# Kernel tuning notes

Measured on AMD Instinct MI355X. Metric: run time of the kernel, lower is better.

The kernel has to match this reference:

```python
import jax, jax.numpy as jnp
import numpy as np

C = 512

def _conv1x1(x, w, b):
    # x: [B, C, T], w: [O, C], b: [O] -> [B, O, T]
    return jnp.einsum('oc,bct->bot', w, x) + b[None, :, None]

def setup_inputs() -> dict:
    key = jax.random.key(0)
    ks = jax.random.split(key, 9)
    B, T = 8, 2048
    s = 1.0 / np.sqrt(C)
    inp = {'x': jax.random.normal(ks[0], (B, C, T), dtype=jnp.float32)}
    names = ['theta', 'phi', 'g', 'w']
    for i, n in enumerate(names):
        inp[f'w_{n}'] = jax.random.uniform(ks[1 + 2 * i], (C, C), jnp.float32, -s, s)
        inp[f'b_{n}'] = jax.random.uniform(ks[2 + 2 * i], (C,), jnp.float32, -s, s)
    return inp

def reference(x, w_theta, b_theta, w_phi, b_phi, w_g, b_g, w_w, b_w):
    relu = jax.nn.relu
    feat_theta = relu(_conv1x1(x, w_theta, b_theta))          # [B, C, T]
    feat_phi = relu(_conv1x1(x, w_phi, b_phi))                # [B, C, T]
    # scores: Q^T K over channel dim -> [B, T, T]
    scores = jnp.einsum('bci,bcj->bij', feat_theta, feat_phi)
    attn = jax.nn.softmax(scores, axis=2)                     # [B, T, T]
    feat_g = relu(_conv1x1(x, w_g, b_g))                      # [B, C, T]
    # attention-weighted V: [B, T, T] x [B, T, C] -> [B, T, C] -> [B, C, T]
    feature = jnp.einsum('bij,bcj->bci', attn, feat_g)
    w_feature = relu(_conv1x1(feature, w_w, b_w))
    return w_feature + x
```

## Files before the change

### kernel.cpp

```cpp
#include <hip/hip_runtime.h>
#include <math.h>

#define C_DIM 512
#define T_DIM 2048
#define B_DIM 8

typedef _Float16 f16;
typedef __attribute__((ext_vector_type(8))) _Float16 half8;
typedef __attribute__((ext_vector_type(4))) _Float16 half4;
typedef __attribute__((ext_vector_type(4))) float floatx4;

__global__ __launch_bounds__(256) void convert_w_kernel(
    const float* __restrict__ w0, const float* __restrict__ w1,
    const float* __restrict__ w2, const float* __restrict__ w3,
    f16* __restrict__ o0, f16* __restrict__ o1,
    f16* __restrict__ o2, f16* __restrict__ o3)
{
    const float* src; f16* dst;
    switch (blockIdx.z) {
        case 0:  src = w0; dst = o0; break;
        case 1:  src = w1; dst = o1; break;
        case 2:  src = w2; dst = o2; break;
        default: src = w3; dst = o3; break;
    }
    const int idx = (blockIdx.x * 256 + threadIdx.x) * 4;
    const float4 v = *(const float4*)(src + idx);
    half4 h; h[0] = (f16)v.x; h[1] = (f16)v.y; h[2] = (f16)v.z; h[3] = (f16)v.w;
    *(half4*)(dst + idx) = h;
}

__global__ __launch_bounds__(256) void concat_bias_kernel(
    const float* __restrict__ b0, const float* __restrict__ b1,
    float* __restrict__ o)
{
    const int i = blockIdx.x * 256 + threadIdx.x;
    o[i] = (i < 512) ? b0[i] : b1[i - 512];
}

__global__ __launch_bounds__(256) void transpose_x_kernel(
    const float* __restrict__ x, f16* __restrict__ xt)
{
    __shared__ float xs[32][33];
    const int b  = blockIdx.z;
    const int t0 = blockIdx.x * 32, c0 = blockIdx.y * 32;
    const float* xb = x + (size_t)b * C_DIM * T_DIM;
    const int r = threadIdx.x >> 3, q = threadIdx.x & 7;

    const float4 v = *(const float4*)(xb + (size_t)(c0 + r) * T_DIM + t0 + q * 4);
    xs[r][q * 4 + 0] = v.x; xs[r][q * 4 + 1] = v.y;
    xs[r][q * 4 + 2] = v.z; xs[r][q * 4 + 3] = v.w;
    __syncthreads();

    f16* xtb = xt + (size_t)b * C_DIM * T_DIM;
    half4 h;
    h[0] = (f16)xs[q * 4 + 0][r]; h[1] = (f16)xs[q * 4 + 1][r];
    h[2] = (f16)xs[q * 4 + 2][r]; h[3] = (f16)xs[q * 4 + 3][r];
    *(half4*)(xtb + (size_t)(t0 + r) * C_DIM + c0 + q * 4) = h;
}

template<int MODE>
__global__ __launch_bounds__(256) void gemm_tn(
    const f16* __restrict__ A, size_t sA, int lda,
    const f16* __restrict__ B, size_t sB, int ldb,
    void* __restrict__ Cp, size_t sC, int ldc,
    const float* __restrict__ bias,
    const float* __restrict__ resid, size_t sR,
    int K)
{
    __shared__ __align__(16) f16 As[2][128 * 32];
    __shared__ __align__(16) f16 Bs[2][128 * 32];

    const int gx = gridDim.x;
    const int flat = blockIdx.y * gx + blockIdx.x;
    const int jsc = gx >> 2;
    const int sh = (jsc <= 1) ? 0 : (31 - __builtin_clz(jsc));
    const int s = flat >> 4, rem = flat & 15;
    const int i0 = ((s >> sh) * 4 + (rem >> 2)) * 128;
    const int j0 = (((jsc <= 1) ? 0 : (s & (jsc - 1))) * 4 + (rem & 3)) * 128;

    const int bz = blockIdx.z;
    A += (size_t)bz * sA;
    B += (size_t)bz * sB;

    const int tid  = threadIdx.x;
    const int lane = tid & 63;
    const int wave = tid >> 6;
    const int wy = wave >> 1, wx = wave & 1;
    const int quad = lane >> 4, l16 = lane & 15;

    const int row1 = tid >> 2, ch = tid & 3;
    const int row2 = row1 + 64;
    const int w1 = row1 * 32 + ((ch ^ (row1 & 3)) << 3);
    const int w2 = row2 * 32 + ((ch ^ (row2 & 3)) << 3);

    const f16* gA1 = A + (size_t)(i0 + row1) * lda + ch * 8;
    const f16* gA2 = A + (size_t)(i0 + row2) * lda + ch * 8;
    const f16* gB1 = B + (size_t)(j0 + row1) * ldb + ch * 8;
    const f16* gB2 = B + (size_t)(j0 + row2) * ldb + ch * 8;

    const int xa = (quad ^ (l16 & 3)) << 3;

    const int nt = K >> 5;

    float4 a1_0 = *(const float4*)(gA1);      float4 a2_0 = *(const float4*)(gA2);
    float4 b1_0 = *(const float4*)(gB1);      float4 b2_0 = *(const float4*)(gB2);
    float4 a1_1 = *(const float4*)(gA1 + 32); float4 a2_1 = *(const float4*)(gA2 + 32);
    float4 b1_1 = *(const float4*)(gB1 + 32); float4 b2_1 = *(const float4*)(gB2 + 32);

    floatx4 acc[4][4] = {};

    for (int t = 0; t < nt; t += 2) {
        *(float4*)&As[0][w1] = a1_0;
        *(float4*)&As[0][w2] = a2_0;
        *(float4*)&Bs[0][w1] = b1_0;
        *(float4*)&Bs[0][w2] = b2_0;
        if (t + 2 < nt) {
            const int off = (t + 2) * 32;
            a1_0 = *(const float4*)(gA1 + off); a2_0 = *(const float4*)(gA2 + off);
            b1_0 = *(const float4*)(gB1 + off); b2_0 = *(const float4*)(gB2 + off);
        }
        __syncthreads();
        {
            half8 af[4], bf[4];
            #pragma unroll
            for (int mi = 0; mi < 4; ++mi)
                af[mi] = *(const half8*)&As[0][(wy * 64 + mi * 16 + l16) * 32 + xa];
            #pragma unroll
            for (int ni = 0; ni < 4; ++ni)
                bf[ni] = *(const half8*)&Bs[0][(wx * 64 + ni * 16 + l16) * 32 + xa];
            #pragma unroll
            for (int mi = 0; mi < 4; ++mi)
                #pragma unroll
                for (int ni = 0; ni < 4; ++ni)
                    acc[mi][ni] = __builtin_amdgcn_mfma_f32_16x16x32_f16(
                        af[mi], bf[ni], acc[mi][ni], 0, 0, 0);
        }
        *(float4*)&As[1][w1] = a1_1;
        *(float4*)&As[1][w2] = a2_1;
        *(float4*)&Bs[1][w1] = b1_1;
        *(float4*)&Bs[1][w2] = b2_1;
        if (t + 3 < nt) {
            const int off = (t + 3) * 32;
            a1_1 = *(const float4*)(gA1 + off); a2_1 = *(const float4*)(gA2 + off);
            b1_1 = *(const float4*)(gB1 + off); b2_1 = *(const float4*)(gB2 + off);
        }
        __syncthreads();
        {
            half8 af[4], bf[4];
            #pragma unroll
            for (int mi = 0; mi < 4; ++mi)
                af[mi] = *(const half8*)&As[1][(wy * 64 + mi * 16 + l16) * 32 + xa];
            #pragma unroll
            for (int ni = 0; ni < 4; ++ni)
                bf[ni] = *(const half8*)&Bs[1][(wx * 64 + ni * 16 + l16) * 32 + xa];
            #pragma unroll
            for (int mi = 0; mi < 4; ++mi)
                #pragma unroll
                for (int ni = 0; ni < 4; ++ni)
                    acc[mi][ni] = __builtin_amdgcn_mfma_f32_16x16x32_f16(
                        af[mi], bf[ni], acc[mi][ni], 0, 0, 0);
        }
    }

    #pragma unroll
    for (int mi = 0; mi < 4; ++mi) {
        #pragma unroll
        for (int ni = 0; ni < 4; ++ni) {
            const int col = j0 + wx * 64 + ni * 16 + l16;
            #pragma unroll
            for (int r = 0; r < 4; ++r) {
                const int row = i0 + wy * 64 + mi * 16 + quad * 4 + r;
                float v = acc[mi][ni][r];
                if (MODE == 1) { v += bias[col]; v = v > 0.f ? v : 0.f; }
                if (MODE == 2) { v += bias[row]; v = v > 0.f ? v : 0.f; }
                if (MODE == 3) {
                    v += bias[row];
                    v = v > 0.f ? v : 0.f;
                    v += resid[(size_t)bz * sR + (size_t)row * ldc + col];
                    ((float*)Cp)[(size_t)bz * sC + (size_t)row * ldc + col] = v;
                } else {
                    ((f16*)Cp)[(size_t)bz * sC + (size_t)row * ldc + col] = (f16)v;
                }
            }
        }
    }
}

__device__ __forceinline__ void gl16(const f16* g, f16* l)
{
    __builtin_amdgcn_global_load_lds(
        (const __attribute__((address_space(1))) unsigned int*)g,
        (__attribute__((address_space(3))) unsigned int*)l,
        16, 0, 0);
}

template<int MODE>
__global__ __launch_bounds__(512, 2) void gemm256(
    const f16* __restrict__ A, size_t sA, int lda,
    const f16* __restrict__ B, size_t sB, int ldb,
    void* __restrict__ Cp, size_t sC, int ldc,
    const float* __restrict__ bias,
    int K)
{
    __shared__ __align__(16) f16 As[2][2][256 * 32];
    __shared__ __align__(16) f16 Bs[2][2][256 * 32];

    const int gx = gridDim.x;
    const int flat = blockIdx.y * gx + blockIdx.x;
    const int jsc = gx >> 2;
    const int sh = (jsc <= 1) ? 0 : (31 - __builtin_clz(jsc));
    const int s = flat >> 4, rem = flat & 15;
    const int i0 = ((s >> sh) * 4 + (rem >> 2)) * 256;
    const int j0 = (((jsc <= 1) ? 0 : (s & (jsc - 1))) * 4 + (rem & 3)) * 256;

    const int bz = blockIdx.z;
    A += (size_t)bz * sA;
    B += (size_t)bz * sB;

    const int tid  = threadIdx.x;
    const int lane = tid & 63;
    const int wave = tid >> 6;
    const int wy = wave >> 2;
    const int wx = wave & 3;
    const int quad = lane >> 4, l16 = lane & 15;

    const int srow = wave * 32 + (lane >> 2);
    const int sch  = lane & 3;
    const f16* gA0 = A + (size_t)(i0 + srow) * lda + sch * 8;
    const f16* gA1 = gA0 + (size_t)16 * lda;
    const f16* gB0 = B + (size_t)(j0 + srow) * ldb + sch * 8;
    const f16* gB1 = gB0 + (size_t)16 * ldb;
    const int wsg = wave * 1024;

    const int ra = (wy * 128 + l16) * 32 + quad * 8;
    const int rb = (wx * 64 + l16) * 32 + quad * 8;

    const int nt = K >> 6;

#define STAGE_A(t, q) do {                                                    \
        const int off_ = (t) * 64 + (q) * 32;                                 \
        gl16(gA0 + off_, &As[(t) & 1][q][wsg]);                               \
        gl16(gA1 + off_, &As[(t) & 1][q][wsg + 512]);                         \
    } while (0)
#define STAGE_B(t, q) do {                                                    \
        const int off_ = (t) * 64 + (q) * 32;                                 \
        gl16(gB0 + off_, &Bs[(t) & 1][q][wsg]);                               \
        gl16(gB1 + off_, &Bs[(t) & 1][q][wsg + 512]);                         \
    } while (0)
#define PH_MFMA(B0) do {                                                      \
        __builtin_amdgcn_s_setprio(1);                                        \
        _Pragma("unroll")                                                     \
        for (int mi = 0; mi < 4; ++mi) {                                      \
            _Pragma("unroll")                                                 \
            for (int ni = 0; ni < 4; ++ni)                                    \
                acc[(B0) + mi][ni] = __builtin_amdgcn_mfma_f32_16x16x32_f16(  \
                    af[mi], bf[ni], acc[(B0) + mi][ni], 0, 0, 0);             \
        }                                                                     \
        __builtin_amdgcn_s_setprio(0);                                        \
    } while (0)

    STAGE_A(0, 0); STAGE_B(0, 0);
    STAGE_A(0, 1); STAGE_B(0, 1);
    STAGE_A(1, 0); STAGE_B(1, 0);

    floatx4 acc[8][4] = {};

    for (int t = 0; t < nt; ++t) {
        const f16* sa0 = &As[t & 1][0][0];
        const f16* sb0 = &Bs[t & 1][0][0];
        const f16* sa1 = &As[t & 1][1][0];
        const f16* sb1 = &Bs[t & 1][1][0];
        half8 af[4], bf[4];

        if (t + 1 < nt) asm volatile("s_waitcnt vmcnt(8)\ns_barrier" ::: "memory");
        else            asm volatile("s_waitcnt vmcnt(4)\ns_barrier" ::: "memory");
        #pragma unroll
        for (int ni = 0; ni < 4; ++ni) bf[ni] = *(const half8*)&sb0[rb + ni * 512];
        #pragma unroll
        for (int mi = 0; mi < 4; ++mi) af[mi] = *(const half8*)&sa0[ra + mi * 512];
        if (t + 1 < nt) STAGE_A(t + 1, 1);
        PH_MFMA(0);

        #pragma unroll
        for (int mi = 0; mi < 4; ++mi) af[mi] = *(const half8*)&sa0[ra + 2048 + mi * 512];
        if (t + 1 < nt) STAGE_B(t + 1, 1);
        PH_MFMA(4);

        if (t + 1 < nt) asm volatile("s_waitcnt vmcnt(8)\ns_barrier" ::: "memory");
        else            asm volatile("s_waitcnt vmcnt(0)\ns_barrier" ::: "memory");
        #pragma unroll
        for (int ni = 0; ni < 4; ++ni) bf[ni] = *(const half8*)&sb1[rb + ni * 512];
        #pragma unroll
        for (int mi = 0; mi < 4; ++mi) af[mi] = *(const half8*)&sa1[ra + mi * 512];
        if (t + 2 < nt) STAGE_A(t + 2, 0);
        PH_MFMA(0);

        #pragma unroll
        for (int mi = 0; mi < 4; ++mi) af[mi] = *(const half8*)&sa1[ra + 2048 + mi * 512];
        if (t + 2 < nt) STAGE_B(t + 2, 0);
        PH_MFMA(4);
    }
#undef STAGE_A
#undef STAGE_B
#undef PH_MFMA

    #pragma unroll
    for (int m = 0; m < 8; ++m) {
        #pragma unroll
        for (int ni = 0; ni < 4; ++ni) {
            const int col = j0 + wx * 64 + ni * 16 + l16;
            #pragma unroll
            for (int r = 0; r < 4; ++r) {
                const int row = i0 + wy * 128 + m * 16 + quad * 4 + r;
                float v = acc[m][ni][r];
                if (MODE == 1) { v += bias[col]; v = v > 0.f ? v : 0.f; }
                ((f16*)Cp)[(size_t)bz * sC + (size_t)row * ldc + col] = (f16)v;
            }
        }
    }
}

__global__ __launch_bounds__(256) void softmax_f16_kernel(f16* __restrict__ S)
{
    f16* p = S + (size_t)blockIdx.x * T_DIM;
    const int tid = threadIdx.x;

    half8 hv = *((const half8*)p + tid);
    float v[8];
    float lmax = -1e30f;
    #pragma unroll
    for (int c = 0; c < 8; ++c) { v[c] = (float)hv[c]; lmax = fmaxf(lmax, v[c]); }
    #pragma unroll
    for (int off = 32; off; off >>= 1)
        lmax = fmaxf(lmax, __shfl_down(lmax, off));
    __shared__ float redm[4];
    if ((tid & 63) == 0) redm[tid >> 6] = lmax;
    __syncthreads();
    const float m = fmaxf(fmaxf(redm[0], redm[1]), fmaxf(redm[2], redm[3]));

    float lsum = 0.f;
    #pragma unroll
    for (int c = 0; c < 8; ++c) { v[c] = __expf(v[c] - m); lsum += v[c]; }
    #pragma unroll
    for (int off = 32; off; off >>= 1)
        lsum += __shfl_down(lsum, off);
    __shared__ float reds[4];
    if ((tid & 63) == 0) reds[tid >> 6] = lsum;
    __syncthreads();
    const float inv = 1.f / (reds[0] + reds[1] + reds[2] + reds[3]);

    #pragma unroll
    for (int c = 0; c < 8; ++c) hv[c] = (f16)(v[c] * inv);
    *((half8*)p + tid) = hv;
}

extern "C" void kernel_launch(void* const* d_in, const int* in_sizes, int n_in,
                              void* d_out, int out_size, void* d_ws, size_t ws_size,
                              hipStream_t stream)
{
    const float* x       = (const float*)d_in[0];
    const float* w_theta = (const float*)d_in[1];
    const float* b_theta = (const float*)d_in[2];
    const float* w_phi   = (const float*)d_in[3];
    const float* b_phi   = (const float*)d_in[4];
    const float* w_g     = (const float*)d_in[5];
    const float* b_g     = (const float*)d_in[6];
    const float* w_w     = (const float*)d_in[7];
    const float* b_w     = (const float*)d_in[8];
    float* out = (float*)d_out;

    const size_t FE = (size_t)B_DIM * C_DIM * T_DIM;
    const size_t TC = (size_t)T_DIM * C_DIM;
    const size_t TT = (size_t)T_DIM * T_DIM;

    f16* xt      = (f16*)d_ws;
    f16* wtp     = xt + FE;
    f16* wg_h    = wtp + 524288;
    f16* ww_h    = wg_h + 262144;
    float* btp   = (float*)(ww_h + 262144);
    f16* tp      = (f16*)(btp + 1024);
    f16* g       = tp + (size_t)B_DIM * T_DIM * 1024;
    f16* scores  = g + FE;
    f16* feature = tp;

    const dim3 blk(256);
    const dim3 blk512(512);

    convert_w_kernel<<<dim3(256, 1, 4), blk, 0, stream>>>(
        w_theta, w_phi, w_g, w_w, wtp, wtp + 262144, wg_h, ww_h);
    concat_bias_kernel<<<dim3(4), blk, 0, stream>>>(b_theta, b_phi, btp);
    transpose_x_kernel<<<dim3(T_DIM / 32, C_DIM / 32, B_DIM), blk, 0, stream>>>(x, xt);

    gemm256<1><<<dim3(1024 / 256, T_DIM / 256, B_DIM), blk512, 0, stream>>>(
        xt, TC, C_DIM, wtp, 0, C_DIM, tp, (size_t)T_DIM * 1024, 1024,
        btp, C_DIM);
    gemm_tn<2><<<dim3(T_DIM / 128, C_DIM / 128, B_DIM), blk, 0, stream>>>(
        wg_h, 0, C_DIM, xt, TC, C_DIM, g, TC, T_DIM, b_g, nullptr, 0, C_DIM);
    gemm256<0><<<dim3(T_DIM / 256, T_DIM / 256, B_DIM), blk512, 0, stream>>>(
        tp, (size_t)T_DIM * 1024, 1024, tp + 512, (size_t)T_DIM * 1024, 1024,
        scores, TT, T_DIM, nullptr, C_DIM);
    softmax_f16_kernel<<<dim3(B_DIM * T_DIM), blk, 0, stream>>>(scores);
    gemm_tn<0><<<dim3(C_DIM / 128, T_DIM / 128, B_DIM), blk, 0, stream>>>(
        scores, TT, T_DIM, g, TC, T_DIM, feature, TC, C_DIM, nullptr, nullptr, 0, T_DIM);
    gemm_tn<3><<<dim3(T_DIM / 128, C_DIM / 128, B_DIM), blk, 0, stream>>>(
        ww_h, 0, C_DIM, feature, TC, C_DIM, out, TC, T_DIM, b_w, x, TC, C_DIM);
}
```

Measured before the change: 270.0 us.

## Replace register-staged 128x128 GEMMs with async LDS-load 128x256 kernel; wave-per-row softmax

```diff
diff --git a/kernel.cpp b/kernel.cpp
--- a/kernel.cpp
+++ b/kernel.cpp
@@ -58,8 +58,142 @@
     *(half4*)(xtb + (size_t)(t0 + r) * C_DIM + c0 + q * 4) = h;
 }
 
+__device__ __forceinline__ void gl16(const f16* g, f16* l)
+{
+    __builtin_amdgcn_global_load_lds(
+        (const __attribute__((address_space(1))) unsigned int*)g,
+        (__attribute__((address_space(3))) unsigned int*)l,
+        16, 0, 0);
+}
+
 template<int MODE>
-__global__ __launch_bounds__(256) void gemm_tn(
+__global__ __launch_bounds__(512, 2) void gemm256(
+    const f16* __restrict__ A, size_t sA, int lda,
+    const f16* __restrict__ B, size_t sB, int ldb,
+    void* __restrict__ Cp, size_t sC, int ldc,
+    const float* __restrict__ bias,
+    int K)
+{
+    __shared__ __align__(16) f16 As[2][2][256 * 32];
+    __shared__ __align__(16) f16 Bs[2][2][256 * 32];
+
+    const int gx = gridDim.x;
+    const int flat = blockIdx.y * gx + blockIdx.x;
+    const int jsc = gx >> 2;
+    const int sh = (jsc <= 1) ? 0 : (31 - __builtin_clz(jsc));
+    const int s = flat >> 4, rem = flat & 15;
+    const int i0 = ((s >> sh) * 4 + (rem >> 2)) * 256;
+    const int j0 = (((jsc <= 1) ? 0 : (s & (jsc - 1))) * 4 + (rem & 3)) * 256;
+
+    const int bz = blockIdx.z;
+    A += (size_t)bz * sA;
+    B += (size_t)bz * sB;
+
+    const int tid  = threadIdx.x;
+    const int lane = tid & 63;
+    const int wave = tid >> 6;
+    const int wy = wave >> 2;
+    const int wx = wave & 3;
+    const int quad = lane >> 4, l16 = lane & 15;
+
+    const int srow = wave * 32 + (lane >> 2);
+    const int sch  = lane & 3;
+    const f16* gA0 = A + (size_t)(i0 + srow) * lda + sch * 8;
+    const f16* gA1 = gA0 + (size_t)16 * lda;
+    const f16* gB0 = B + (size_t)(j0 + srow) * ldb + sch * 8;
+    const f16* gB1 = gB0 + (size_t)16 * ldb;
+    const int wsg = wave * 1024;
+
+    const int ra = (wy * 128 + l16) * 32 + quad * 8;
+    const int rb = (wx * 64 + l16) * 32 + quad * 8;
+
+    const int nt = K >> 6;
+
+#define STAGE_A(t, q) do {                                                    \
+        const int off_ = (t) * 64 + (q) * 32;                                 \
+        gl16(gA0 + off_, &As[(t) & 1][q][wsg]);                               \
+        gl16(gA1 + off_, &As[(t) & 1][q][wsg + 512]);                         \
+    } while (0)
+#define STAGE_B(t, q) do {                                                    \
+        const int off_ = (t) * 64 + (q) * 32;                                 \
+        gl16(gB0 + off_, &Bs[(t) & 1][q][wsg]);                               \
+        gl16(gB1 + off_, &Bs[(t) & 1][q][wsg + 512]);                         \
+    } while (0)
+#define PH_MFMA(B0) do {                                                      \
+        __builtin_amdgcn_s_setprio(1);                                        \
+        _Pragma("unroll")                                                     \
+        for (int mi = 0; mi < 4; ++mi) {                                      \
+            _Pragma("unroll")                                                 \
+            for (int ni = 0; ni < 4; ++ni)                                    \
+                acc[(B0) + mi][ni] = __builtin_amdgcn_mfma_f32_16x16x32_f16(  \
+                    af[mi], bf[ni], acc[(B0) + mi][ni], 0, 0, 0);             \
+        }                                                                     \
+        __builtin_amdgcn_s_setprio(0);                                        \
+    } while (0)
+
+    STAGE_A(0, 0); STAGE_B(0, 0);
+    STAGE_A(0, 1); STAGE_B(0, 1);
+    STAGE_A(1, 0); STAGE_B(1, 0);
+
+    floatx4 acc[8][4] = {};
+
+    for (int t = 0; t < nt; ++t) {
+        const f16* sa0 = &As[t & 1][0][0];
+        const f16* sb0 = &Bs[t & 1][0][0];
+        const f16* sa1 = &As[t & 1][1][0];
+        const f16* sb1 = &Bs[t & 1][1][0];
+        half8 af[4], bf[4];
+
+        if (t + 1 < nt) asm volatile("s_waitcnt vmcnt(8)\ns_barrier" ::: "memory");
+        else            asm volatile("s_waitcnt vmcnt(4)\ns_barrier" ::: "memory");
+        #pragma unroll
+        for (int ni = 0; ni < 4; ++ni) bf[ni] = *(const half8*)&sb0[rb + ni * 512];
+        #pragma unroll
+        for (int mi = 0; mi < 4; ++mi) af[mi] = *(const half8*)&sa0[ra + mi * 512];
+        if (t + 1 < nt) STAGE_A(t + 1, 1);
+        PH_MFMA(0);
+
+        #pragma unroll
+        for (int mi = 0; mi < 4; ++mi) af[mi] = *(const half8*)&sa0[ra + 2048 + mi * 512];
+        if (t + 1 < nt) STAGE_B(t + 1, 1);
+        PH_MFMA(4);
+
+        if (t + 1 < nt) asm volatile("s_waitcnt vmcnt(8)\ns_barrier" ::: "memory");
+        else            asm volatile("s_waitcnt vmcnt(0)\ns_barrier" ::: "memory");
+        #pragma unroll
+        for (int ni = 0; ni < 4; ++ni) bf[ni] = *(const half8*)&sb1[rb + ni * 512];
+        #pragma unroll
+        for (int mi = 0; mi < 4; ++mi) af[mi] = *(const half8*)&sa1[ra + mi * 512];
+        if (t + 2 < nt) STAGE_A(t + 2, 0);
+        PH_MFMA(0);
+
+        #pragma unroll
+        for (int mi = 0; mi < 4; ++mi) af[mi] = *(const half8*)&sa1[ra + 2048 + mi * 512];
+        if (t + 2 < nt) STAGE_B(t + 2, 0);
+        PH_MFMA(4);
+    }
+#undef STAGE_A
+#undef STAGE_B
+#undef PH_MFMA
+
+    #pragma unroll
+    for (int m = 0; m < 8; ++m) {
+        #pragma unroll
+        for (int ni = 0; ni < 4; ++ni) {
+            const int col = j0 + wx * 64 + ni * 16 + l16;
+            #pragma unroll
+            for (int r = 0; r < 4; ++r) {
+                const int row = i0 + wy * 128 + m * 16 + quad * 4 + r;
+                float v = acc[m][ni][r];
+                if (MODE == 1) { v += bias[col]; v = v > 0.f ? v : 0.f; }
+                ((f16*)Cp)[(size_t)bz * sC + (size_t)row * ldc + col] = (f16)v;
+            }
+        }
+    }
+}
+
+template<int MODE>
+__global__ __launch_bounds__(512, 2) void gemm_wide(
     const f16* __restrict__ A, size_t sA, int lda,
     const f16* __restrict__ B, size_t sB, int ldb,
     void* __restrict__ Cp, size_t sC, int ldc,
@@ -67,17 +201,11 @@
     const float* __restrict__ resid, size_t sR,
     int K)
 {
-    __shared__ __align__(16) f16 As[2][128 * 32];
-    __shared__ __align__(16) f16 Bs[2][128 * 32];
-
-    const int gx = gridDim.x;
-    const int flat = blockIdx.y * gx + blockIdx.x;
-    const int jsc = gx >> 2;
-    const int sh = (jsc <= 1) ? 0 : (31 - __builtin_clz(jsc));
-    const int s = flat >> 4, rem = flat & 15;
-    const int i0 = ((s >> sh) * 4 + (rem >> 2)) * 128;
-    const int j0 = (((jsc <= 1) ? 0 : (s & (jsc - 1))) * 4 + (rem & 3)) * 128;
-
+    __shared__ __align__(16) f16 As[2][2][128 * 32];
+    __shared__ __align__(16) f16 Bs[2][2][256 * 32];
+
+    const int i0 = blockIdx.y * 128;
+    const int j0 = blockIdx.x * 256;
     const int bz = blockIdx.z;
     A += (size_t)bz * sA;
     B += (size_t)bz * sB;
@@ -85,82 +213,73 @@
     const int tid  = threadIdx.x;
     const int lane = tid & 63;
     const int wave = tid >> 6;
-    const int wy = wave >> 1, wx = wave & 1;
+    const int wy = wave >> 2;
+    const int wx = wave & 3;
     const int quad = lane >> 4, l16 = lane & 15;
 
-    const int row1 = tid >> 2, ch = tid & 3;
-    const int row2 = row1 + 64;
-    const int w1 = row1 * 32 + ((ch ^ (row1 & 3)) << 3);
-    const int w2 = row2 * 32 + ((ch ^ (row2 & 3)) << 3);
-
-    const f16* gA1 = A + (size_t)(i0 + row1) * lda + ch * 8;
-    const f16* gA2 = A + (size_t)(i0 + row2) * lda + ch * 8;
-    const f16* gB1 = B + (size_t)(j0 + row1) * ldb + ch * 8;
-    const f16* gB2 = B + (size_t)(j0 + row2) * ldb + ch * 8;
-
-    const int xa = (quad ^ (l16 & 3)) << 3;
-
-    const int nt = K >> 5;
-
-    float4 a1_0 = *(const float4*)(gA1);      float4 a2_0 = *(const float4*)(gA2);
-    float4 b1_0 = *(const float4*)(gB1);      float4 b2_0 = *(const float4*)(gB2);
-    float4 a1_1 = *(const float4*)(gA1 + 32); float4 a2_1 = *(const float4*)(gA2 + 32);
-    float4 b1_1 = *(const float4*)(gB1 + 32); float4 b2_1 = *(const float4*)(gB2 + 32);
+    const f16* gA0 = A + (size_t)(i0 + wave * 16 + (lane >> 2)) * lda + (lane & 3) * 8;
+    const f16* gB0 = B + (size_t)(j0 + wave * 32 + (lane >> 2)) * ldb + (lane & 3) * 8;
+    const f16* gB1 = gB0 + (size_t)16 * ldb;
+
+    const int ra = (wy * 64 + l16) * 32 + quad * 8;
+    const int rb = (wx * 64 + l16) * 32 + quad * 8;
+
+    const int nt = K >> 6;
+
+#define WSTAGE_A(t, q) do {                                                   \
+        gl16(gA0 + (t) * 64 + (q) * 32, &As[(t) & 1][q][wave * 512]);         \
+    } while (0)
+#define WSTAGE_B(t, q) do {                                                   \
+        const int off_ = (t) * 64 + (q) * 32;                                 \
+        gl16(gB0 + off_, &Bs[(t) & 1][q][wave * 1024]);                       \
+        gl16(gB1 + off_, &Bs[(t) & 1][q][wave * 1024 + 512]);                 \
+    } while (0)
+#define WPH_MFMA() do {                                                       \
+        __builtin_amdgcn_s_setprio(1);                                        \
+        _Pragma("unroll")                                                     \
+        for (int mi = 0; mi < 4; ++mi) {                                      \
+            _Pragma("unroll")                                                 \
+            for (int ni = 0; ni < 4; ++ni)                                    \
+                acc[mi][ni] = __builtin_amdgcn_mfma_f32_16x16x32_f16(         \
+                    af[mi], bf[ni], acc[mi][ni], 0, 0, 0);                    \
+        }                                                                     \
+        __builtin_amdgcn_s_setprio(0);                                        \
+    } while (0)
+
+    WSTAGE_A(0, 0); WSTAGE_B(0, 0);
+    WSTAGE_A(0, 1); WSTAGE_B(0, 1);
+    WSTAGE_A(1, 0); WSTAGE_B(1, 0);
 
     floatx4 acc[4][4] = {};
 
-    for (int t = 0; t < nt; t += 2) {
-        *(float4*)&As[0][w1] = a1_0;
-        *(float4*)&As[0][w2] = a2_0;
-        *(float4*)&Bs[0][w1] = b1_0;
-        *(float4*)&Bs[0][w2] = b2_0;
-        if (t + 2 < nt) {
-            const int off = (t + 2) * 32;
-            a1_0 = *(const float4*)(gA1 + off); a2_0 = *(const float4*)(gA2 + off);
-            b1_0 = *(const float4*)(gB1 + off); b2_0 = *(const float4*)(gB2 + off);
-        }
-        __syncthreads();
-        {
-            half8 af[4], bf[4];
-            #pragma unroll
-            for (int mi = 0; mi < 4; ++mi)
-                af[mi] = *(const half8*)&As[0][(wy * 64 + mi * 16 + l16) * 32 + xa];
-            #pragma unroll
-            for (int ni = 0; ni < 4; ++ni)
-                bf[ni] = *(const half8*)&Bs[0][(wx * 64 + ni * 16 + l16) * 32 + xa];
-            #pragma unroll
-            for (int mi = 0; mi < 4; ++mi)
-                #pragma unroll
-                for (int ni = 0; ni < 4; ++ni)
-                    acc[mi][ni] = __builtin_amdgcn_mfma_f32_16x16x32_f16(
-                        af[mi], bf[ni], acc[mi][ni], 0, 0, 0);
-        }
-        *(float4*)&As[1][w1] = a1_1;
-        *(float4*)&As[1][w2] = a2_1;
-        *(float4*)&Bs[1][w1] = b1_1;
-        *(float4*)&Bs[1][w2] = b2_1;
-        if (t + 3 < nt) {
-            const int off = (t + 3) * 32;
-            a1_1 = *(const float4*)(gA1 + off); a2_1 = *(const float4*)(gA2 + off);
-            b1_1 = *(const float4*)(gB1 + off); b2_1 = *(const float4*)(gB2 + off);
-        }
-        __syncthreads();
-        {
-            half8 af[4], bf[4];
-            #pragma unroll
-            for (int mi = 0; mi < 4; ++mi)
-                af[mi] = *(const half8*)&As[1][(wy * 64 + mi * 16 + l16) * 32 + xa];
-            #pragma unroll
-            for (int ni = 0; ni < 4; ++ni)
-                bf[ni] = *(const half8*)&Bs[1][(wx * 64 + ni * 16 + l16) * 32 + xa];
-            #pragma unroll
-            for (int mi = 0; mi < 4; ++mi)
-                #pragma unroll
-                for (int ni = 0; ni < 4; ++ni)
-                    acc[mi][ni] = __builtin_amdgcn_mfma_f32_16x16x32_f16(
-                        af[mi], bf[ni], acc[mi][ni], 0, 0, 0);
-        }
-    }
+    for (int t = 0; t < nt; ++t) {
+        const f16* sa0 = &As[t & 1][0][0];
+        const f16* sb0 = &Bs[t & 1][0][0];
+        const f16* sa1 = &As[t & 1][1][0];
+        const f16* sb1 = &Bs[t & 1][1][0];
+        half8 af[4], bf[4];
+
+        if (t + 1 < nt) asm volatile("s_waitcnt vmcnt(6)\ns_barrier" ::: "memory");
+        else            asm volatile("s_waitcnt vmcnt(3)\ns_barrier" ::: "memory");
+        #pragma unroll
+        for (int ni = 0; ni < 4; ++ni) bf[ni] = *(const half8*)&sb0[rb + ni * 512];
+        #pragma unroll
+        for (int mi = 0; mi < 4; ++mi) af[mi] = *(const half8*)&sa0[ra + mi * 512];
+        if (t + 1 < nt) { WSTAGE_A(t + 1, 1); WSTAGE_B(t + 1, 1); }
+        WPH_MFMA();
+
+        if (t + 1 < nt) asm volatile("s_waitcnt vmcnt(6)\ns_barrier" ::: "memory");
+        else            asm volatile("s_waitcnt vmcnt(0)\ns_barrier" ::: "memory");
+        #pragma unroll
+        for (int ni = 0; ni < 4; ++ni) bf[ni] = *(const half8*)&sb1[rb + ni * 512];
+        #pragma unroll
+        for (int mi = 0; mi < 4; ++mi) af[mi] = *(const half8*)&sa1[ra + mi * 512];
+        if (t + 2 < nt) { WSTAGE_A(t + 2, 0); WSTAGE_B(t + 2, 0); }
+        WPH_MFMA();
+    }
+#undef WSTAGE_A
+#undef WSTAGE_B
+#undef WPH_MFMA
 
     #pragma unroll
     for (int mi = 0; mi < 4; ++mi) {
@@ -171,7 +290,6 @@
             for (int r = 0; r < 4; ++r) {
                 const int row = i0 + wy * 64 + mi * 16 + quad * 4 + r;
                 float v = acc[mi][ni][r];
-                if (MODE == 1) { v += bias[col]; v = v > 0.f ? v : 0.f; }
                 if (MODE == 2) { v += bias[row]; v = v > 0.f ? v : 0.f; }
                 if (MODE == 3) {
                     v += bias[row];
@@ -186,172 +304,39 @@
     }
 }
 
-__device__ __forceinline__ void gl16(const f16* g, f16* l)
-{
-    __builtin_amdgcn_global_load_lds(
-        (const __attribute__((address_space(1))) unsigned int*)g,
-        (__attribute__((address_space(3))) unsigned int*)l,
-        16, 0, 0);
-}
-
-template<int MODE>
-__global__ __launch_bounds__(512, 2) void gemm256(
-    const f16* __restrict__ A, size_t sA, int lda,
-    const f16* __restrict__ B, size_t sB, int ldb,
-    void* __restrict__ Cp, size_t sC, int ldc,
-    const float* __restrict__ bias,
-    int K)
-{
-    __shared__ __align__(16) f16 As[2][2][256 * 32];
-    __shared__ __align__(16) f16 Bs[2][2][256 * 32];
-
-    const int gx = gridDim.x;
-    const int flat = blockIdx.y * gx + blockIdx.x;
-    const int jsc = gx >> 2;
-    const int sh = (jsc <= 1) ? 0 : (31 - __builtin_clz(jsc));
-    const int s = flat >> 4, rem = flat & 15;
-    const int i0 = ((s >> sh) * 4 + (rem >> 2)) * 256;
-    const int j0 = (((jsc <= 1) ? 0 : (s & (jsc - 1))) * 4 + (rem & 3)) * 256;
-
-    const int bz = blockIdx.z;
-    A += (size_t)bz * sA;
-    B += (size_t)bz * sB;
-
-    const int tid  = threadIdx.x;
-    const int lane = tid & 63;
-    const int wave = tid >> 6;
-    const int wy = wave >> 2;
-    const int wx = wave & 3;
-    const int quad = lane >> 4, l16 = lane & 15;
-
-    const int srow = wave * 32 + (lane >> 2);
-    const int sch  = lane & 3;
-    const f16* gA0 = A + (size_t)(i0 + srow) * lda + sch * 8;
-    const f16* gA1 = gA0 + (size_t)16 * lda;
-    const f16* gB0 = B + (size_t)(j0 + srow) * ldb + sch * 8;
-    const f16* gB1 = gB0 + (size_t)16 * ldb;
-    const int wsg = wave * 1024;
-
-    const int ra = (wy * 128 + l16) * 32 + quad * 8;
-    const int rb = (wx * 64 + l16) * 32 + quad * 8;
-
-    const int nt = K >> 6;
-
-#define STAGE_A(t, q) do {                                                    \
-        const int off_ = (t) * 64 + (q) * 32;                                 \
-        gl16(gA0 + off_, &As[(t) & 1][q][wsg]);                               \
-        gl16(gA1 + off_, &As[(t) & 1][q][wsg + 512]);                         \
-    } while (0)
-#define STAGE_B(t, q) do {                                                    \
-        const int off_ = (t) * 64 + (q) * 32;                                 \
-        gl16(gB0 + off_, &Bs[(t) & 1][q][wsg]);                               \
-        gl16(gB1 + off_, &Bs[(t) & 1][q][wsg + 512]);                         \
-    } while (0)
-#define PH_MFMA(B0) do {                                                      \
-        __builtin_amdgcn_s_setprio(1);                                        \
-        _Pragma("unroll")                                                     \
-        for (int mi = 0; mi < 4; ++mi) {                                      \
-            _Pragma("unroll")                                                 \
-            for (int ni = 0; ni < 4; ++ni)                                    \
-                acc[(B0) + mi][ni] = __builtin_amdgcn_mfma_f32_16x16x32_f16(  \
-                    af[mi], bf[ni], acc[(B0) + mi][ni], 0, 0, 0);             \
-        }                                                                     \
-        __builtin_amdgcn_s_setprio(0);                                        \
-    } while (0)
-
-    STAGE_A(0, 0); STAGE_B(0, 0);
-    STAGE_A(0, 1); STAGE_B(0, 1);
-    STAGE_A(1, 0); STAGE_B(1, 0);
-
-    floatx4 acc[8][4] = {};
-
-    for (int t = 0; t < nt; ++t) {
-        const f16* sa0 = &As[t & 1][0][0];
-        const f16* sb0 = &Bs[t & 1][0][0];
-        const f16* sa1 = &As[t & 1][1][0];
-        const f16* sb1 = &Bs[t & 1][1][0];
-        half8 af[4], bf[4];
-
-        if (t + 1 < nt) asm volatile("s_waitcnt vmcnt(8)\ns_barrier" ::: "memory");
-        else            asm volatile("s_waitcnt vmcnt(4)\ns_barrier" ::: "memory");
-        #pragma unroll
-        for (int ni = 0; ni < 4; ++ni) bf[ni] = *(const half8*)&sb0[rb + ni * 512];
-        #pragma unroll
-        for (int mi = 0; mi < 4; ++mi) af[mi] = *(const half8*)&sa0[ra + mi * 512];
-        if (t + 1 < nt) STAGE_A(t + 1, 1);
-        PH_MFMA(0);
-
-        #pragma unroll
-        for (int mi = 0; mi < 4; ++mi) af[mi] = *(const half8*)&sa0[ra + 2048 + mi * 512];
-        if (t + 1 < nt) STAGE_B(t + 1, 1);
-        PH_MFMA(4);
-
-        if (t + 1 < nt) asm volatile("s_waitcnt vmcnt(8)\ns_barrier" ::: "memory");
-        else            asm volatile("s_waitcnt vmcnt(0)\ns_barrier" ::: "memory");
-        #pragma unroll
-        for (int ni = 0; ni < 4; ++ni) bf[ni] = *(const half8*)&sb1[rb + ni * 512];
-        #pragma unroll
-        for (int mi = 0; mi < 4; ++mi) af[mi] = *(const half8*)&sa1[ra + mi * 512];
-        if (t + 2 < nt) STAGE_A(t + 2, 0);
-        PH_MFMA(0);
-
-        #pragma unroll
-        for (int mi = 0; mi < 4; ++mi) af[mi] = *(const half8*)&sa1[ra + 2048 + mi * 512];
-        if (t + 2 < nt) STAGE_B(t + 2, 0);
-        PH_MFMA(4);
-    }
-#undef STAGE_A
-#undef STAGE_B
-#undef PH_MFMA
-
-    #pragma unroll
-    for (int m = 0; m < 8; ++m) {
-        #pragma unroll
-        for (int ni = 0; ni < 4; ++ni) {
-            const int col = j0 + wx * 64 + ni * 16 + l16;
-            #pragma unroll
-            for (int r = 0; r < 4; ++r) {
-                const int row = i0 + wy * 128 + m * 16 + quad * 4 + r;
-                float v = acc[m][ni][r];
-                if (MODE == 1) { v += bias[col]; v = v > 0.f ? v : 0.f; }
-                ((f16*)Cp)[(size_t)bz * sC + (size_t)row * ldc + col] = (f16)v;
-            }
+__global__ __launch_bounds__(256) void softmax_f16_kernel(f16* __restrict__ S)
+{
+    const int lane = threadIdx.x & 63;
+    f16* p = S + (size_t)(blockIdx.x * 4 + (threadIdx.x >> 6)) * T_DIM;
+
+    half8 h[4];
+    float v[32];
+    float m = -1e30f;
+    #pragma unroll
+    for (int u = 0; u < 4; ++u) {
+        h[u] = *((const half8*)p + (u * 64 + lane));
+        #pragma unroll
+        for (int c = 0; c < 8; ++c) {
+            v[u * 8 + c] = (float)h[u][c];
+            m = fmaxf(m, v[u * 8 + c]);
         }
     }
-}
-
-__global__ __launch_bounds__(256) void softmax_f16_kernel(f16* __restrict__ S)
-{
-    f16* p = S + (size_t)blockIdx.x * T_DIM;
-    const int tid = threadIdx.x;
-
-    half8 hv = *((const half8*)p + tid);
-    float v[8];
-    float lmax = -1e30f;
-    #pragma unroll
-    for (int c = 0; c < 8; ++c) { v[c] = (float)hv[c]; lmax = fmaxf(lmax, v[c]); }
-    #pragma unroll
-    for (int off = 32; off; off >>= 1)
-        lmax = fmaxf(lmax, __shfl_down(lmax, off));
-    __shared__ float redm[4];
-    if ((tid & 63) == 0) redm[tid >> 6] = lmax;
-    __syncthreads();
-    const float m = fmaxf(fmaxf(redm[0], redm[1]), fmaxf(redm[2], redm[3]));
-
-    float lsum = 0.f;
-    #pragma unroll
-    for (int c = 0; c < 8; ++c) { v[c] = __expf(v[c] - m); lsum += v[c]; }
-    #pragma unroll
-    for (int off = 32; off; off >>= 1)
-        lsum += __shfl_down(lsum, off);
-    __shared__ float reds[4];
-    if ((tid & 63) == 0) reds[tid >> 6] = lsum;
-    __syncthreads();
-    const float inv = 1.f / (reds[0] + reds[1] + reds[2] + reds[3]);
-
-    #pragma unroll
-    for (int c = 0; c < 8; ++c) hv[c] = (f16)(v[c] * inv);
-    *((half8*)p + tid) = hv;
+    #pragma unroll
+    for (int off = 32; off; off >>= 1) m = fmaxf(m, __shfl_xor(m, off));
+
+    float s = 0.f;
+    #pragma unroll
+    for (int i = 0; i < 32; ++i) { v[i] = __expf(v[i] - m); s += v[i]; }
+    #pragma unroll
+    for (int off = 32; off; off >>= 1) s += __shfl_xor(s, off);
+    const float inv = 1.f / s;
+
+    #pragma unroll
+    for (int u = 0; u < 4; ++u) {
+        #pragma unroll
+        for (int c = 0; c < 8; ++c) h[u][c] = (f16)(v[u * 8 + c] * inv);
+        *((half8*)p + (u * 64 + lane)) = h[u];
+    }
 }
 
 extern "C" void kernel_launch(void* const* d_in, const int* in_sizes, int n_in,
@@ -394,14 +379,15 @@
     gemm256<1><<<dim3(1024 / 256, T_DIM / 256, B_DIM), blk512, 0, stream>>>(
         xt, TC, C_DIM, wtp, 0, C_DIM, tp, (size_t)T_DIM * 1024, 1024,
         btp, C_DIM);
-    gemm_tn<2><<<dim3(T_DIM / 128, C_DIM / 128, B_DIM), blk, 0, stream>>>(
+    gemm_wide<2><<<dim3(T_DIM / 256, C_DIM / 128, B_DIM), blk512, 0, stream>>>(
         wg_h, 0, C_DIM, xt, TC, C_DIM, g, TC, T_DIM, b_g, nullptr, 0, C_DIM);
     gemm256<0><<<dim3(T_DIM / 256, T_DIM / 256, B_DIM), blk512, 0, stream>>>(
         tp, (size_t)T_DIM * 1024, 1024, tp + 512, (size_t)T_DIM * 1024, 1024,
         scores, TT, T_DIM, nullptr, C_DIM);
-    softmax_f16_kernel<<<dim3(B_DIM * T_DIM), blk, 0, stream>>>(scores);
-    gemm_tn<0><<<dim3(C_DIM / 128, T_DIM / 128, B_DIM), blk, 0, stream>>>(
-        scores, TT, T_DIM, g, TC, T_DIM, feature, TC, C_DIM, nullptr, nullptr, 0, T_DIM);
-    gemm_tn<3><<<dim3(T_DIM / 128, C_DIM / 128, B_DIM), blk, 0, stream>>>(
+    softmax_f16_kernel<<<dim3(B_DIM * T_DIM / 4), blk, 0, stream>>>(scores);
+    gemm_wide<0><<<dim3(C_DIM / 256, T_DIM / 128, B_DIM), blk512, 0, stream>>>(
+        scores, TT, T_DIM, g, TC, T_DIM, feature, TC, C_DIM,
+        nullptr, nullptr, 0, T_DIM);
+    gemm_wide<3><<<dim3(T_DIM / 256, C_DIM / 128, B_DIM), blk512, 0, stream>>>(
         ww_h, 0, C_DIM, feature, TC, C_DIM, out, TC, T_DIM, b_w, x, TC, C_DIM);
 }
```

Measured after the change: 271.5 us. No clear change (+0.6%).
